# Kernel optimization log

Hardware: AMD Instinct MI355X
Metric: run time of the kernel (lower is better)

Reference implementation:

```python
import jax, jax.numpy as jnp
import numpy as np

N = 100000
DIM = 128
N_EDGES = 3200000
EPS = 1e-5


def setup_inputs() -> dict:
    key = jax.random.key(0)
    k1, k2, k3, k4, k5, k6 = jax.random.split(key, 6)
    x = jax.random.normal(k1, (N, DIM), dtype=jnp.float32)
    edge_row = jnp.sort(jax.random.randint(k2, (N_EDGES,), 0, N, dtype=jnp.int64))
    edge_col = jax.random.randint(k3, (N_EDGES,), 0, N, dtype=jnp.int64)
    edge_val = jax.random.uniform(k4, (N_EDGES,), dtype=jnp.float32)
    gamma = jnp.ones((DIM,), dtype=jnp.float32)
    beta = jnp.zeros((DIM,), dtype=jnp.float32)
    return {"x": x, "edge_row": edge_row, "edge_col": edge_col,
            "edge_val": edge_val, "gamma": gamma, "beta": beta}


def _layernorm(h, gamma, beta):
    mu = jnp.mean(h, axis=-1, keepdims=True)
    var = jnp.mean(jnp.square(h - mu), axis=-1, keepdims=True)
    return (h - mu) * jax.lax.rsqrt(var + EPS) * gamma + beta


def reference(x, edge_row, edge_col, edge_val, gamma, beta):
    # sparse adj @ x  ==  segment-sum of val * x[src] into dst rows
    msgs = edge_val[:, None] * x[edge_col]            # [E, DIM]
    h = jax.ops.segment_sum(msgs, edge_row, num_segments=N)  # [N, DIM]
    return _layernorm(h + x, gamma, beta)
```

## Files before the change

### kernel.cpp

```cpp
#include <hip/hip_runtime.h>
#include <hip/hip_fp16.h>

#define DIM 128
#define EPS 1e-5f
#define WPB 4
#define EPQ 8

typedef float vfloat2 __attribute__((ext_vector_type(2)));

__global__ void quant_kernel(const float4* __restrict__ x4,
                             unsigned int* __restrict__ x8,
                             float*        __restrict__ scales,
                             int n_nodes)
{
    const int t   = blockIdx.x * blockDim.x + threadIdx.x;
    const int row = t >> 5;
    if (row >= n_nodes) return;

    const float4 v = x4[t];
    float m = fmaxf(fmaxf(fabsf(v.x), fabsf(v.y)),
                    fmaxf(fabsf(v.z), fabsf(v.w)));
#pragma unroll
    for (int off = 1; off <= 16; off <<= 1)
        m = fmaxf(m, __shfl_xor(m, off, 64));

    const float inv = (m > 0.f) ? 127.f / m : 0.f;
    const int q0 = __float2int_rn(v.x * inv) + 128;
    const int q1 = __float2int_rn(v.y * inv) + 128;
    const int q2 = __float2int_rn(v.z * inv) + 128;
    const int q3 = __float2int_rn(v.w * inv) + 128;
    x8[t] = (unsigned)q0 | ((unsigned)q1 << 8) |
            ((unsigned)q2 << 16) | ((unsigned)q3 << 24);

    if ((threadIdx.x & 31) == 0)
        scales[row] = m * (1.f / 127.f);
}

__global__ void csr_kernel(const int* __restrict__ edge_row,
                           int* __restrict__ row_ptr,
                           int n_nodes, int n_edges)
{
    int i = blockIdx.x * blockDim.x + threadIdx.x;
    if (i >= n_edges) return;
    int cur  = edge_row[i];
    int prev = (i == 0) ? -1 : edge_row[i - 1];
    for (int r = prev + 1; r <= cur; ++r) row_ptr[r] = i;
    if (i == n_edges - 1) {
        for (int r = cur + 1; r <= n_nodes; ++r) row_ptr[r] = n_edges;
    }
}

__global__ __launch_bounds__(WPB * 64)
void gnn_fused_kernel(const uint2* __restrict__ x8,
                      const float* __restrict__ scales,
                      const int*   __restrict__ row_ptr,
                      const int*   __restrict__ edge_col,
                      const float* __restrict__ edge_val,
                      const float* __restrict__ gamma,
                      const float* __restrict__ beta,
                      float*       __restrict__ out,
                      int n_nodes, int n_edges)
{
    const int wave = threadIdx.x >> 6;
    const int lane = threadIdx.x & 63;
    const int q    = lane >> 4;
    const int sub  = lane & 15;
    const int node = blockIdx.x * WPB + wave;
    if (node >= n_nodes) return;

    const int start = row_ptr[node];
    const int end   = row_ptr[node + 1];
    const unsigned len = (unsigned)(end - start);

    const uint2 xr = x8[node * (DIM / 8) + sub];
    const float sn = scales[node];

    float acc[8];
#pragma unroll
    for (int k = 0; k < 8; ++k) acc[k] = 0.f;
    float Kws = 0.f;

    const int ebase = start & ~3;
    const int emax  = n_edges - 4;
    for (int e0 = ebase; e0 < end; e0 += 4 * EPQ) {
        const int b  = e0 + EPQ * q;
        const int b0 = min(b, emax);
        const int b1 = min(b + 4, emax);
        int4   c4a = *(const int4*)  (edge_col + b0);
        int4   c4b = *(const int4*)  (edge_col + b1);
        float4 w4a = *(const float4*)(edge_val + b0);
        float4 w4b = *(const float4*)(edge_val + b1);

        int   c[EPQ] = {c4a.x, c4a.y, c4a.z, c4a.w,
                        c4b.x, c4b.y, c4b.z, c4b.w};
        float w[EPQ] = {w4a.x, w4a.y, w4a.z, w4a.w,
                        w4b.x, w4b.y, w4b.z, w4b.w};

        const int off = b - start;
#pragma unroll
        for (int u = 0; u < EPQ; ++u) {
            bool in = (unsigned)(off + u) < len;
            c[u] = in ? c[u] : 0;
            w[u] = in ? w[u] : 0.f;
        }

        float ws[EPQ];
#pragma unroll
        for (int u = 0; u < EPQ; ++u)
            ws[u] = w[u] * scales[c[u]];

        uint2 v[EPQ];
#pragma unroll
        for (int u = 0; u < EPQ; ++u)
            v[u] = x8[c[u] * (DIM / 8) + sub];

#pragma unroll
        for (int u = 0; u < EPQ; ++u) {
            const unsigned lo = v[u].x, hi = v[u].y;
            Kws += ws[u];
            acc[0] = fmaf(ws[u], (float)( lo        & 0xffu), acc[0]);
            acc[1] = fmaf(ws[u], (float)((lo >>  8) & 0xffu), acc[1]);
            acc[2] = fmaf(ws[u], (float)((lo >> 16) & 0xffu), acc[2]);
            acc[3] = fmaf(ws[u], (float)( lo >> 24        ), acc[3]);
            acc[4] = fmaf(ws[u], (float)( hi        & 0xffu), acc[4]);
            acc[5] = fmaf(ws[u], (float)((hi >>  8) & 0xffu), acc[5]);
            acc[6] = fmaf(ws[u], (float)((hi >> 16) & 0xffu), acc[6]);
            acc[7] = fmaf(ws[u], (float)( hi >> 24        ), acc[7]);
        }
    }

#pragma unroll
    for (int k = 0; k < 8; ++k)
        acc[k] = fmaf(-128.f, Kws, acc[k]);

#pragma unroll
    for (int k = 0; k < 8; ++k) {
        acc[k] += __shfl_xor(acc[k], 16, 64);
        acc[k] += __shfl_xor(acc[k], 32, 64);
    }

    const float r0 = -128.f * sn;
    const unsigned rlo = xr.x, rhi = xr.y;
    float h[8];
    h[0] = acc[0] + fmaf(sn, (float)( rlo        & 0xffu), r0);
    h[1] = acc[1] + fmaf(sn, (float)((rlo >>  8) & 0xffu), r0);
    h[2] = acc[2] + fmaf(sn, (float)((rlo >> 16) & 0xffu), r0);
    h[3] = acc[3] + fmaf(sn, (float)( rlo >> 24        ), r0);
    h[4] = acc[4] + fmaf(sn, (float)( rhi        & 0xffu), r0);
    h[5] = acc[5] + fmaf(sn, (float)((rhi >>  8) & 0xffu), r0);
    h[6] = acc[6] + fmaf(sn, (float)((rhi >> 16) & 0xffu), r0);
    h[7] = acc[7] + fmaf(sn, (float)( rhi >> 24        ), r0);

    float s = 0.f, sq = 0.f;
#pragma unroll
    for (int k = 0; k < 8; ++k) { s += h[k]; sq += h[k] * h[k]; }
#pragma unroll
    for (int off = 1; off <= 8; off <<= 1) {
        s  += __shfl_xor(s,  off, 64);
        sq += __shfl_xor(sq, off, 64);
    }
    const float mean = s * (1.0f / (float)DIM);
    const float var  = sq * (1.0f / (float)DIM) - mean * mean;
    const float rs   = rsqrtf(var + EPS);

    float hx = (q < 2) ? ((q == 0) ? h[0] : h[2]) : ((q == 2) ? h[4] : h[6]);
    float hy = (q < 2) ? ((q == 0) ? h[1] : h[3]) : ((q == 2) ? h[5] : h[7]);
    const int didx = sub * 4 + q;
    const float2 g = ((const float2*)gamma)[didx];
    const float2 b = ((const float2*)beta)[didx];
    vfloat2 o;
    o.x = (hx - mean) * rs * g.x + b.x;
    o.y = (hy - mean) * rs * g.y + b.y;
    __builtin_nontemporal_store(o, (vfloat2*)out + node * (DIM / 2) + didx);
}

extern "C" void kernel_launch(void* const* d_in, const int* in_sizes, int n_in,
                              void* d_out, int out_size, void* d_ws, size_t ws_size,
                              hipStream_t stream)
{
    const float* x        = (const float*)d_in[0];
    const int*   edge_row = (const int*)  d_in[1];
    const int*   edge_col = (const int*)  d_in[2];
    const float* edge_val = (const float*)d_in[3];
    const float* gamma    = (const float*)d_in[4];
    const float* beta     = (const float*)d_in[5];
    float*       out      = (float*)d_out;

    const int n_nodes = in_sizes[0] / DIM;
    const int n_edges = in_sizes[1];
    const int n_elem  = in_sizes[0];

    unsigned int* x8      = (unsigned int*)d_ws;
    int*          row_ptr = (int*)  ((char*)d_ws + (size_t)n_elem);
    float*        scales  = (float*)((char*)d_ws + (size_t)n_elem
                                     + (size_t)(n_nodes + 1) * sizeof(int));

    const int qthreads = n_nodes * (DIM / 4);
    quant_kernel<<<(qthreads + 255) / 256, 256, 0, stream>>>(
        (const float4*)x, x8, scales, n_nodes);
    csr_kernel<<<(n_edges + 255) / 256, 256, 0, stream>>>(
        edge_row, row_ptr, n_nodes, n_edges);

    const int blocks = (n_nodes + WPB - 1) / WPB;
    gnn_fused_kernel<<<blocks, WPB * 64, 0, stream>>>(
        (const uint2*)x8, scales, row_ptr, edge_col, edge_val,
        gamma, beta, out, n_nodes, n_edges);
}
```

Baseline: 224.1 us.

## Precompute fp16 per-edge scaled weights and split edge loop into masked/unmasked trips

The per-edge product of edge value and source-node scale is now computed once in the CSR-building kernel and stored as fp16. This removes the scattered scales gather from the main SpMM loop and halves weight bandwidth there. The main edge loop now takes 4 edges per quarter-wave instead of 8, with masking applied only to the first and last trips. The trade-offs are an extra gather of the scale array in the CSR kernel, fp16 rounding of the weights, and less memory-level parallelism per iteration.

```diff
diff --git a/kernel.cpp b/kernel.cpp
--- a/kernel.cpp
+++ b/kernel.cpp
@@ -4,7 +4,7 @@
 #define DIM 128
 #define EPS 1e-5f
 #define WPB 4
-#define EPQ 8
+#define UF  4
 
 typedef float vfloat2 __attribute__((ext_vector_type(2)));
 
@@ -36,12 +36,19 @@
         scales[row] = m * (1.f / 127.f);
 }
 
-__global__ void csr_kernel(const int* __restrict__ edge_row,
-                           int* __restrict__ row_ptr,
-                           int n_nodes, int n_edges)
+__global__ void csr_scale_kernel(const int*   __restrict__ edge_row,
+                                 const int*   __restrict__ edge_col,
+                                 const float* __restrict__ edge_val,
+                                 const float* __restrict__ scales,
+                                 int*         __restrict__ row_ptr,
+                                 __half*      __restrict__ wsh,
+                                 int n_nodes, int n_edges)
 {
     int i = blockIdx.x * blockDim.x + threadIdx.x;
     if (i >= n_edges) return;
+
+    wsh[i] = __float2half(edge_val[i] * scales[edge_col[i]]);
+
     int cur  = edge_row[i];
     int prev = (i == 0) ? -1 : edge_row[i - 1];
     for (int r = prev + 1; r <= cur; ++r) row_ptr[r] = i;
@@ -50,12 +57,61 @@
     }
 }
 
+template<bool MASKED>
+__device__ __forceinline__
+void edge_trip(int e0, int q, int sub, int start, unsigned len, int emax,
+               const uint2* __restrict__ x8,
+               const int*   __restrict__ edge_col,
+               const __half* __restrict__ wsh,
+               float acc[8], float& Kws)
+{
+    const int b  = e0 + 4 * q;
+    const int bc = MASKED ? min(b, emax) : b;
+    int4    c4 = *(const int4*)   (edge_col + bc);
+    ushort4 wv = *(const ushort4*)((const unsigned short*)wsh + bc);
+
+    int c[UF] = {c4.x, c4.y, c4.z, c4.w};
+    const __half* hw = (const __half*)&wv;
+    float w[UF];
+#pragma unroll
+    for (int u = 0; u < UF; ++u) w[u] = __half2float(hw[u]);
+
+    if (MASKED) {
+        const int off = b - start;
+#pragma unroll
+        for (int u = 0; u < UF; ++u) {
+            bool in = (unsigned)(off + u) < len;
+            c[u] = in ? c[u] : 0;
+            w[u] = in ? w[u] : 0.f;
+        }
+    }
+
+    uint2 v[UF];
+#pragma unroll
+    for (int u = 0; u < UF; ++u)
+        v[u] = x8[c[u] * (DIM / 8) + sub];
+
+#pragma unroll
+    for (int u = 0; u < UF; ++u) {
+        const unsigned lo = v[u].x, hi = v[u].y;
+        Kws += w[u];
+        acc[0] = fmaf(w[u], (float)( lo        & 0xffu), acc[0]);
+        acc[1] = fmaf(w[u], (float)((lo >>  8) & 0xffu), acc[1]);
+        acc[2] = fmaf(w[u], (float)((lo >> 16) & 0xffu), acc[2]);
+        acc[3] = fmaf(w[u], (float)( lo >> 24        ), acc[3]);
+        acc[4] = fmaf(w[u], (float)( hi        & 0xffu), acc[4]);
+        acc[5] = fmaf(w[u], (float)((hi >>  8) & 0xffu), acc[5]);
+        acc[6] = fmaf(w[u], (float)((hi >> 16) & 0xffu), acc[6]);
+        acc[7] = fmaf(w[u], (float)( hi >> 24        ), acc[7]);
+    }
+}
+
 __global__ __launch_bounds__(WPB * 64)
 void gnn_fused_kernel(const uint2* __restrict__ x8,
                       const float* __restrict__ scales,
                       const int*   __restrict__ row_ptr,
                       const int*   __restrict__ edge_col,
-                      const float* __restrict__ edge_val,
+                      const __half* __restrict__ wsh,
                       const float* __restrict__ gamma,
                       const float* __restrict__ beta,
                       float*       __restrict__ out,
@@ -82,51 +138,17 @@
 
     const int ebase = start & ~3;
     const int emax  = n_edges - 4;
-    for (int e0 = ebase; e0 < end; e0 += 4 * EPQ) {
-        const int b  = e0 + EPQ * q;
-        const int b0 = min(b, emax);
-        const int b1 = min(b + 4, emax);
-        int4   c4a = *(const int4*)  (edge_col + b0);
-        int4   c4b = *(const int4*)  (edge_col + b1);
-        float4 w4a = *(const float4*)(edge_val + b0);
-        float4 w4b = *(const float4*)(edge_val + b1);
-
-        int   c[EPQ] = {c4a.x, c4a.y, c4a.z, c4a.w,
-                        c4b.x, c4b.y, c4b.z, c4b.w};
-        float w[EPQ] = {w4a.x, w4a.y, w4a.z, w4a.w,
-                        w4b.x, w4b.y, w4b.z, w4b.w};
-
-        const int off = b - start;
-#pragma unroll
-        for (int u = 0; u < EPQ; ++u) {
-            bool in = (unsigned)(off + u) < len;
-            c[u] = in ? c[u] : 0;
-            w[u] = in ? w[u] : 0.f;
-        }
-
-        float ws[EPQ];
-#pragma unroll
-        for (int u = 0; u < EPQ; ++u)
-            ws[u] = w[u] * scales[c[u]];
-
-        uint2 v[EPQ];
-#pragma unroll
-        for (int u = 0; u < EPQ; ++u)
-            v[u] = x8[c[u] * (DIM / 8) + sub];
-
-#pragma unroll
-        for (int u = 0; u < EPQ; ++u) {
-            const unsigned lo = v[u].x, hi = v[u].y;
-            Kws += ws[u];
-            acc[0] = fmaf(ws[u], (float)( lo        & 0xffu), acc[0]);
-            acc[1] = fmaf(ws[u], (float)((lo >>  8) & 0xffu), acc[1]);
-            acc[2] = fmaf(ws[u], (float)((lo >> 16) & 0xffu), acc[2]);
-            acc[3] = fmaf(ws[u], (float)( lo >> 24        ), acc[3]);
-            acc[4] = fmaf(ws[u], (float)( hi        & 0xffu), acc[4]);
-            acc[5] = fmaf(ws[u], (float)((hi >>  8) & 0xffu), acc[5]);
-            acc[6] = fmaf(ws[u], (float)((hi >> 16) & 0xffu), acc[6]);
-            acc[7] = fmaf(ws[u], (float)( hi >> 24        ), acc[7]);
-        }
+
+    if (ebase < end) {
+        edge_trip<true>(ebase, q, sub, start, len, emax,
+                        x8, edge_col, wsh, acc, Kws);
+        int e0 = ebase + 4 * UF;
+        for (; e0 + 4 * UF <= end; e0 += 4 * UF)
+            edge_trip<false>(e0, q, sub, start, len, emax,
+                             x8, edge_col, wsh, acc, Kws);
+        if (e0 < end)
+            edge_trip<true>(e0, q, sub, start, len, emax,
+                            x8, edge_col, wsh, acc, Kws);
     }
 
 #pragma unroll
@@ -190,19 +212,23 @@
     const int n_edges = in_sizes[1];
     const int n_elem  = in_sizes[0];
 
-    unsigned int* x8      = (unsigned int*)d_ws;
-    int*          row_ptr = (int*)  ((char*)d_ws + (size_t)n_elem);
-    float*        scales  = (float*)((char*)d_ws + (size_t)n_elem
+    unsigned char* wsb = (unsigned char*)d_ws;
+    unsigned int* x8      = (unsigned int*)wsb;
+    int*          row_ptr = (int*)  (wsb + (size_t)n_elem);
+    float*        scales  = (float*)(wsb + (size_t)n_elem
                                      + (size_t)(n_nodes + 1) * sizeof(int));
+    size_t wsh_off = ((size_t)n_elem + (size_t)(n_nodes + 1) * sizeof(int)
+                      + (size_t)n_nodes * sizeof(float) + 15) & ~(size_t)15;
+    __half*       wsh     = (__half*)(wsb + wsh_off);
 
     const int qthreads = n_nodes * (DIM / 4);
     quant_kernel<<<(qthreads + 255) / 256, 256, 0, stream>>>(
         (const float4*)x, x8, scales, n_nodes);
-    csr_kernel<<<(n_edges + 255) / 256, 256, 0, stream>>>(
-        edge_row, row_ptr, n_nodes, n_edges);
+    csr_scale_kernel<<<(n_edges + 255) / 256, 256, 0, stream>>>(
+        edge_row, edge_col, edge_val, scales, row_ptr, wsh, n_nodes, n_edges);
 
     const int blocks = (n_nodes + WPB - 1) / WPB;
     gnn_fused_kernel<<<blocks, WPB * 64, 0, stream>>>(
-        (const uint2*)x8, scales, row_ptr, edge_col, edge_val,
+        (const uint2*)x8, scales, row_ptr, edge_col, wsh,
         gamma, beta, out, n_nodes, n_edges);
 }
```

Measured after the change: 218.4 us. 2.5% less time.
